# Kernel tuning notes

Hardware: AMD Instinct MI355X
Metric: run time of the kernel (lower is better)

The kernel has to match this reference:

```python
import jax, jax.numpy as jnp
import numpy as np

EPS_PHI = 1e-18  # weight assigned to neighbors outside the support radius


def setup_inputs() -> dict:
    key = jax.random.key(0)
    k1, k2, k3, k4 = jax.random.split(key, 4)
    N, P, K = 2, 100000, 60
    points = jax.random.normal(k1, (N, P, 3), dtype=jnp.float32)
    v = jax.random.normal(k2, (N, P, K, 3), dtype=jnp.float32)
    vn = jax.random.normal(k3, (N, P, K, 3), dtype=jnp.float32)
    # squared support radii: positive, bounded away from zero
    sr = jax.random.uniform(k4, (N, P, K), dtype=jnp.float32) + 0.1
    return {"points": points, "v": v, "vn": vn, "sr": sr}


def reference(points, v, vn, sr):
    # points: (N,P,3); v,vn: (N,P,K,3); sr: (N,P,K)
    p_v = points[:, :, None, :] - v                      # (N,P,K,3)
    dists = jnp.sum(p_v * p_v, axis=-1)                  # (N,P,K) squared distances
    inside = dists < sr                                  # (N,P,K)
    w = 1.0 - dists / sr
    phi_v = jnp.where(inside, (w * w) * (w * w), EPS_PHI)  # quartic kernel weight
    v_to_p_dot_n = jnp.sum(vn * p_v, axis=-1)            # (N,P,K)
    sdf = jnp.sum(phi_v * v_to_p_dot_n, axis=-1) / jnp.sum(phi_v, axis=-1)  # (N,P)
    return jnp.sum(sdf * sdf, axis=-1)                   # (N,)
```

## Files before the change

### kernel.cpp

```cpp
#include <hip/hip_runtime.h>

#define RED_THREADS 512

__global__ __launch_bounds__(256) void sdf_main(
    const float* __restrict__ points,
    const float* __restrict__ v,
    const float* __restrict__ vn,
    const float* __restrict__ sr,
    float* __restrict__ ws,
    int NP, int P, int slots, int slotStride)
{
    constexpr int K = 60;
    __shared__ float4 sv[4][45];
    __shared__ float4 sn[4][45];
    __shared__ float4 ss[4][15];

    const int w     = threadIdx.x >> 6;
    const int lane  = threadIdx.x & 63;
    const int point = blockIdx.x * 4 + w;
    const bool active = point < NP;

    float px = 0.f, py = 0.f, pz = 0.f;
    if (active) {
        const float4* v4 = (const float4*)(v  + (size_t)point * (K * 3));
        const float4* n4 = (const float4*)(vn + (size_t)point * (K * 3));
        const float4* s4 = (const float4*)(sr + (size_t)point * K);
        float4 rv, rn, rs;
        if (lane < 45) rv = v4[lane];
        if (lane < 45) rn = n4[lane];
        if (lane < 15) rs = s4[lane];
        px = points[point * 3 + 0];
        py = points[point * 3 + 1];
        pz = points[point * 3 + 2];
        if (lane < 45) sv[w][lane] = rv;
        if (lane < 45) sn[w][lane] = rn;
        if (lane < 15) ss[w][lane] = rs;
    }
    __syncthreads();

    float num = 0.f, den = 0.f;
    if (active && lane < K) {
        const float* vf = (const float*)sv[w];
        const float* nf = (const float*)sn[w];
        const float* sf = (const float*)ss[w];
        const float vx = vf[3 * lane + 0];
        const float vy = vf[3 * lane + 1];
        const float vz = vf[3 * lane + 2];
        const float nx = nf[3 * lane + 0];
        const float ny = nf[3 * lane + 1];
        const float nz = nf[3 * lane + 2];
        const float s  = sf[lane];

        const float dx = px - vx;
        const float dy = py - vy;
        const float dz = pz - vz;
        const float d2 = dx * dx + dy * dy + dz * dz;
        const float wq = 1.0f - d2 / s;
        const float w2 = wq * wq;
        const float phi = (d2 < s) ? (w2 * w2) : 1e-18f;
        const float dot = nx * dx + ny * dy + nz * dz;
        num = phi * dot;
        den = phi;
    }

    #pragma unroll
    for (int off = 32; off >= 1; off >>= 1) {
        num += __shfl_xor(num, off, 64);
        den += __shfl_xor(den, off, 64);
    }

    if (active && lane == 0) {
        const float sdf = num / den;
        const int n    = point / P;
        const int slot = point & (slots - 1);
        atomicAdd(&ws[slot * slotStride + n], sdf * sdf);
    }
}

__global__ __launch_bounds__(RED_THREADS) void sdf_reduce(
    const float* __restrict__ ws, float* __restrict__ out,
    int N, int slots, int slotStride)
{
    __shared__ float sm0[RED_THREADS];
    __shared__ float sm1[RED_THREADS];
    const int tid = threadIdx.x;
    float a = 0.f, b = 0.f;
    for (int s = tid; s < slots; s += RED_THREADS) {
        a += ws[s * slotStride + 0];
        if (N > 1) b += ws[s * slotStride + 1];
    }
    sm0[tid] = a;
    sm1[tid] = b;
    __syncthreads();
    #pragma unroll
    for (int s = RED_THREADS / 2; s >= 1; s >>= 1) {
        if (tid < s) {
            sm0[tid] += sm0[tid + s];
            sm1[tid] += sm1[tid + s];
        }
        __syncthreads();
    }
    if (tid == 0) {
        out[0] = sm0[0];
        if (N > 1) out[1] = sm1[0];
    }
}

extern "C" void kernel_launch(void* const* d_in, const int* in_sizes, int n_in,
                              void* d_out, int out_size, void* d_ws, size_t ws_size,
                              hipStream_t stream) {
    const float* points = (const float*)d_in[0];
    const float* v      = (const float*)d_in[1];
    const float* vn     = (const float*)d_in[2];
    const float* sr     = (const float*)d_in[3];
    float* out = (float*)d_out;
    float* ws  = (float*)d_ws;

    const int NP = in_sizes[0] / 3;
    const int N  = out_size;
    const int P  = NP / N;

    int slots = 512, slotStride = 16;
    if (ws_size < (size_t)(slots * slotStride * sizeof(float))) {
        slots = 256; slotStride = 2;
    }

    hipMemsetAsync(ws, 0, (size_t)slots * slotStride * sizeof(float), stream);

    const int blocks = (NP + 3) / 4;
    sdf_main<<<blocks, 256, 0, stream>>>(points, v, vn, sr, ws, NP, P,
                                         slots, slotStride);
    sdf_reduce<<<1, RED_THREADS, 0, stream>>>(ws, out, N, slots, slotStride);
}
```

Baseline: 328.6 us.

## Use persistent grid-stride waves with register prefetch and per-wave accumulation

Replaces one-block-per-four-points with a persistent grid of at most 2048 blocks. Each wave loops over points with a grid stride and prefetches the next point's data into registers while computing the current one. The LDS staging and __syncthreads are dropped, and each lane reads its own strided floats directly, which gives uncoalesced 12-byte-stride loads. Per-wave partial sums replace one atomic per point. The trade-off is less memory-level parallelism per wave and non-vectorized loads, against fewer blocks and fewer atomics. The batch split assumes N<=2.

```diff
diff --git a/kernel.cpp b/kernel.cpp
--- a/kernel.cpp
+++ b/kernel.cpp
@@ -8,72 +8,84 @@
     const float* __restrict__ vn,
     const float* __restrict__ sr,
     float* __restrict__ ws,
-    int NP, int P, int slots, int slotStride)
+    int NP, int P, int totalWaves, int slots, int slotStride)
 {
     constexpr int K = 60;
-    __shared__ float4 sv[4][45];
-    __shared__ float4 sn[4][45];
-    __shared__ float4 ss[4][15];
+    const int lane = threadIdx.x & 63;
+    const int wid  = blockIdx.x * 4 + (threadIdx.x >> 6);
+    const bool lk  = lane < K;
 
-    const int w     = threadIdx.x >> 6;
-    const int lane  = threadIdx.x & 63;
-    const int point = blockIdx.x * 4 + w;
-    const bool active = point < NP;
+    const int stride   = totalWaves;
+    const size_t vstep = (size_t)stride * (K * 3);
+    const size_t sstep = (size_t)stride * K;
+    const size_t pstep = (size_t)stride * 3;
 
-    float px = 0.f, py = 0.f, pz = 0.f;
-    if (active) {
-        const float4* v4 = (const float4*)(v  + (size_t)point * (K * 3));
-        const float4* n4 = (const float4*)(vn + (size_t)point * (K * 3));
-        const float4* s4 = (const float4*)(sr + (size_t)point * K);
-        float4 rv, rn, rs;
-        if (lane < 45) rv = v4[lane];
-        if (lane < 45) rn = n4[lane];
-        if (lane < 15) rs = s4[lane];
-        px = points[point * 3 + 0];
-        py = points[point * 3 + 1];
-        pz = points[point * 3 + 2];
-        if (lane < 45) sv[w][lane] = rv;
-        if (lane < 45) sn[w][lane] = rn;
-        if (lane < 15) ss[w][lane] = rs;
-    }
-    __syncthreads();
+    int pt = wid;
+    bool have = pt < NP;
 
-    float num = 0.f, den = 0.f;
-    if (active && lane < K) {
-        const float* vf = (const float*)sv[w];
-        const float* nf = (const float*)sn[w];
-        const float* sf = (const float*)ss[w];
-        const float vx = vf[3 * lane + 0];
-        const float vy = vf[3 * lane + 1];
-        const float vz = vf[3 * lane + 2];
-        const float nx = nf[3 * lane + 0];
-        const float ny = nf[3 * lane + 1];
-        const float nz = nf[3 * lane + 2];
-        const float s  = sf[lane];
+    const float* vp = v      + (size_t)pt * (K * 3) + 3 * lane;
+    const float* qp = vn     + (size_t)pt * (K * 3) + 3 * lane;
+    const float* sp = sr     + (size_t)pt * K       + lane;
+    const float* pp = points + (size_t)pt * 3;
 
-        const float dx = px - vx;
-        const float dy = py - vy;
-        const float dz = pz - vz;
-        const float d2 = dx * dx + dy * dy + dz * dz;
-        const float wq = 1.0f - d2 / s;
-        const float w2 = wq * wq;
-        const float phi = (d2 < s) ? (w2 * w2) : 1e-18f;
-        const float dot = nx * dx + ny * dy + nz * dz;
-        num = phi * dot;
-        den = phi;
+    float cvx = 0.f, cvy = 0.f, cvz = 0.f;
+    float cnx = 0.f, cny = 0.f, cnz = 0.f, cs = 1.f;
+    float cpx = 0.f, cpy = 0.f, cpz = 0.f;
+    if (have) {
+        if (lk) {
+            cvx = vp[0]; cvy = vp[1]; cvz = vp[2];
+            cnx = qp[0]; cny = qp[1]; cnz = qp[2];
+            cs  = sp[0];
+        }
+        cpx = pp[0]; cpy = pp[1]; cpz = pp[2];
     }
 
-    #pragma unroll
-    for (int off = 32; off >= 1; off >>= 1) {
-        num += __shfl_xor(num, off, 64);
-        den += __shfl_xor(den, off, 64);
+    float acc0 = 0.f, acc1 = 0.f;
+
+    while (have) {
+        const bool haveN = (pt + stride) < NP;
+        float nvx = 0.f, nvy = 0.f, nvz = 0.f;
+        float nnx = 0.f, nny = 0.f, nnz = 0.f, ns = 1.f;
+        float npx = 0.f, npy = 0.f, npz = 0.f;
+        if (haveN) {
+            if (lk) {
+                nvx = vp[vstep + 0]; nvy = vp[vstep + 1]; nvz = vp[vstep + 2];
+                nnx = qp[vstep + 0]; nny = qp[vstep + 1]; nnz = qp[vstep + 2];
+                ns  = sp[sstep];
+            }
+            npx = pp[pstep + 0]; npy = pp[pstep + 1]; npz = pp[pstep + 2];
+        }
+
+        const float dx = cpx - cvx;
+        const float dy = cpy - cvy;
+        const float dz = cpz - cvz;
+        const float d2 = dx * dx + dy * dy + dz * dz;
+        const float wq = 1.0f - d2 / cs;
+        const float w2 = wq * wq;
+        const float phi = (d2 < cs) ? (w2 * w2) : 1e-18f;
+        const float dot = cnx * dx + cny * dy + cnz * dz;
+        float num = lk ? (phi * dot) : 0.f;
+        float den = lk ? phi : 0.f;
+        #pragma unroll
+        for (int off = 32; off >= 1; off >>= 1) {
+            num += __shfl_xor(num, off, 64);
+            den += __shfl_xor(den, off, 64);
+        }
+        const float sdf = num / den;
+        const float s2  = sdf * sdf;
+        if (pt < P) acc0 += s2; else acc1 += s2;
+
+        cvx = nvx; cvy = nvy; cvz = nvz;
+        cnx = nnx; cny = nny; cnz = nnz; cs = ns;
+        cpx = npx; cpy = npy; cpz = npz;
+        vp += vstep; qp += vstep; sp += sstep; pp += pstep;
+        pt += stride; have = haveN;
     }
 
-    if (active && lane == 0) {
-        const float sdf = num / den;
-        const int n    = point / P;
-        const int slot = point & (slots - 1);
-        atomicAdd(&ws[slot * slotStride + n], sdf * sdf);
+    if (lane == 0) {
+        const int slot = wid & (slots - 1);
+        atomicAdd(&ws[slot * slotStride + 0], acc0);
+        atomicAdd(&ws[slot * slotStride + 1], acc1);
     }
 }
 
@@ -127,8 +139,11 @@
 
     hipMemsetAsync(ws, 0, (size_t)slots * slotStride * sizeof(float), stream);
 
-    const int blocks = (NP + 3) / 4;
+    int blocks = (NP + 3) / 4;
+    if (blocks > 2048) blocks = 2048;
+    const int totalWaves = blocks * 4;
+
     sdf_main<<<blocks, 256, 0, stream>>>(points, v, vn, sr, ws, NP, P,
-                                         slots, slotStride);
+                                         totalWaves, slots, slotStride);
     sdf_reduce<<<1, RED_THREADS, 0, stream>>>(ws, out, N, slots, slotStride);
 }
```

Measured after the change: 336.0 us. +2.3%, slower.
